# Optimization experiments

Hardware: AMD Instinct MI355X
Metric: run time of the kernel (lower is better)

## Reference

```python
import jax, jax.numpy as jnp
import numpy as np

D = 2048
N_HEADS = 16
N_KV = 4
HEAD_DIM = D // N_HEADS  # 128
N_REP = N_HEADS // N_KV  # 4
B, S = 2, 2048


def setup_inputs() -> dict:
    key = jax.random.key(0)
    ks = jax.random.split(key, 5)
    scale = 0.02
    return {
        "x": jax.random.normal(ks[0], (B, S, D), dtype=jnp.float32),
        "wq": jax.random.normal(ks[1], (D, N_HEADS * HEAD_DIM), dtype=jnp.float32) * scale,
        "wk": jax.random.normal(ks[2], (D, N_KV * HEAD_DIM), dtype=jnp.float32) * scale,
        "wv": jax.random.normal(ks[3], (D, N_KV * HEAD_DIM), dtype=jnp.float32) * scale,
        "wo": jax.random.normal(ks[4], (N_HEADS * HEAD_DIM, D), dtype=jnp.float32) * scale,
    }


def reference(x, wq, wk, wv, wo):
    b, s, _ = x.shape
    # projections
    xq = (x @ wq).reshape(b, s, N_HEADS, HEAD_DIM)
    xk = (x @ wk).reshape(b, s, N_KV, HEAD_DIM)
    xv = (x @ wv).reshape(b, s, N_KV, HEAD_DIM)
    # GQA: group queries per kv head -> [b, n_kv, n_rep, s, d]
    xq = xq.transpose(0, 2, 1, 3).reshape(b, N_KV, N_REP, s, HEAD_DIM)
    xk = xk.transpose(0, 2, 1, 3)  # [b, n_kv, s, d]
    xv = xv.transpose(0, 2, 1, 3)
    scale = 1.0 / jnp.sqrt(jnp.asarray(HEAD_DIM, dtype=x.dtype))
    scores = jnp.einsum('bkrqd,bkvd->bkrqv', xq, xk) * scale  # [b,n_kv,n_rep,s,s]
    causal = jnp.triu(jnp.ones((s, s), dtype=bool), k=1)
    scores = jnp.where(causal, jnp.asarray(-jnp.inf, dtype=scores.dtype), scores)
    probs = jax.nn.softmax(scores, axis=-1)
    out = jnp.einsum('bkrqv,bkvd->bkrqd', probs, xv)  # [b,n_kv,n_rep,s,d]
    out = out.reshape(b, N_HEADS, s, HEAD_DIM).transpose(0, 2, 1, 3).reshape(b, s, N_HEADS * HEAD_DIM)
    return out @ wo
```

## Files before the change

kernel.cpp:

```cpp
#include <hip/hip_runtime.h>

typedef unsigned short u16;
using bf16x8 = __attribute__((ext_vector_type(8))) short;
using bf16x4 = __attribute__((ext_vector_type(4))) short;
using f32x4  = __attribute__((ext_vector_type(4))) float;

#define ATTN_NEG (-3.0e38f)

#if __has_builtin(__builtin_amdgcn_mfma_f32_16x16x16_bf16)
__device__ __forceinline__ f32x4 mfma16(bf16x4 a, bf16x4 b, f32x4 c) {
  return __builtin_amdgcn_mfma_f32_16x16x16_bf16(a, b, c, 0, 0, 0);
}
#elif __has_builtin(__builtin_amdgcn_mfma_f32_16x16x16bf16_1k)
__device__ __forceinline__ f32x4 mfma16(bf16x4 a, bf16x4 b, f32x4 c) {
  return __builtin_amdgcn_mfma_f32_16x16x16bf16_1k(a, b, c, 0, 0, 0);
}
#else
__device__ __forceinline__ f32x4 mfma16(bf16x4 a, bf16x4 b, f32x4 c) {
  asm volatile("v_mfma_f32_16x16x16_bf16 %0, %1, %2, %3"
               : "=v"(c) : "v"(a), "v"(b), "v"(c));
  return c;
}
#endif

__device__ __forceinline__ u16 f2bf_rne(float f) {
  unsigned int u = __float_as_uint(f);
  u += 0x7fffu + ((u >> 16) & 1u);
  return (u16)(u >> 16);
}

__device__ __forceinline__ void load_lds16(const u16* g, u16* l) {
  using gp = const __attribute__((address_space(1))) unsigned int*;
  using lp = __attribute__((address_space(3))) unsigned int*;
  __builtin_amdgcn_global_load_lds((gp)g, (lp)l, 16, 0, 0);
}

__device__ __forceinline__ void transpose_body(const float* __restrict__ in,
                                               u16* __restrict__ out, int K, int N,
                                               int bx, int by, int tid) {
  __shared__ float tile[32][33];
  int tx = tid & 31, ty = tid >> 5;
  int x0 = bx * 32, y0 = by * 32;
  #pragma unroll
  for (int i = 0; i < 32; i += 8)
    tile[ty + i][tx] = in[(size_t)(y0 + ty + i) * N + x0 + tx];
  __syncthreads();
  #pragma unroll
  for (int i = 0; i < 32; i += 8)
    out[(size_t)(x0 + ty + i) * K + y0 + tx] = f2bf_rne(tile[tx][ty + i]);
}

__global__ __launch_bounds__(256) void prep_kernel(const float* __restrict__ x,
                                                   const float* __restrict__ wq,
                                                   const float* __restrict__ wk,
                                                   const float* __restrict__ wv,
                                                   const float* __restrict__ wo,
                                                   u16* xb, u16* wqt, u16* wkt, u16* wvt,
                                                   u16* wot) {
  int bid = blockIdx.x, tid = threadIdx.x;
  if (bid < 8192) {
    int i = bid * 1024 + tid * 4;
    float4 v = *(const float4*)(x + i);
    u16* p = xb + i;
    p[0] = f2bf_rne(v.x); p[1] = f2bf_rne(v.y); p[2] = f2bf_rne(v.z); p[3] = f2bf_rne(v.w);
  } else if (bid < 12288) {
    int t = bid - 8192;
    transpose_body(wq, wqt, 2048, 2048, t & 63, t >> 6, tid);
  } else if (bid < 13312) {
    int t = bid - 12288;
    transpose_body(wk, wkt, 2048, 512, t & 15, t >> 4, tid);
  } else if (bid < 14336) {
    int t = bid - 13312;
    transpose_body(wv, wvt, 2048, 512, t & 15, t >> 4, tid);
  } else {
    int t = bid - 14336;
    transpose_body(wo, wot, 2048, 2048, t & 63, t >> 6, tid);
  }
}

template <int MODE>
__device__ __forceinline__ void gemm_tile(const u16* __restrict__ A, const u16* __restrict__ Bt,
                                          void* __restrict__ Cv, int M, int N, int K,
                                          int bx, int by, char* smem) {
  u16* As = (u16*)smem;
  u16* Bs = (u16*)(smem + 16384);
  const int tid  = threadIdx.x;
  const int wave = tid >> 6, lane = tid & 63;
  const int quad = lane >> 4, l16 = lane & 15;
  const int m0 = by * 128, n0 = bx * 128;
  const int wm = (wave >> 1) * 64, wn = (wave & 1) * 64;
  f32x4 acc[4][4] = {};

  const int srow = lane >> 2;
  const int scol = (lane & 3) << 3;

  for (int k0 = 0; k0 < K; k0 += 64) {
    __syncthreads();
    #pragma unroll
    for (int h = 0; h < 2; ++h)
      #pragma unroll
      for (int i = 0; i < 2; ++i) {
        const int row = wave * 16 + i * 64;
        load_lds16(A  + (size_t)(m0 + row + srow) * K + k0 + h * 32 + scol,
                   As + h * 4096 + row * 32);
        load_lds16(Bt + (size_t)(n0 + row + srow) * K + k0 + h * 32 + scol,
                   Bs + h * 4096 + row * 32);
      }
    __syncthreads();
    #pragma unroll
    for (int h = 0; h < 2; ++h) {
      bf16x8 af[4], bfr[4];
      #pragma unroll
      for (int i = 0; i < 4; ++i) {
        af[i]  = *(const bf16x8*)(As + h * 4096 + (wm + i * 16 + l16) * 32 + quad * 8);
        bfr[i] = *(const bf16x8*)(Bs + h * 4096 + (wn + i * 16 + l16) * 32 + quad * 8);
      }
      #pragma unroll
      for (int mi = 0; mi < 4; ++mi)
        #pragma unroll
        for (int ni = 0; ni < 4; ++ni)
          acc[mi][ni] =
              __builtin_amdgcn_mfma_f32_16x16x32_bf16(af[mi], bfr[ni], acc[mi][ni], 0, 0, 0);
    }
  }

  if constexpr (MODE == 0 || MODE == 3) {
    const float sc = (MODE == 3) ? 0.12751742f : 1.0f;
    u16* Cb = (u16*)Cv;
    #pragma unroll
    for (int mi = 0; mi < 4; ++mi)
      #pragma unroll
      for (int ni = 0; ni < 4; ++ni) {
        int row = m0 + wm + mi * 16 + quad * 4;
        int col = n0 + wn + ni * 16 + l16;
        #pragma unroll
        for (int r = 0; r < 4; ++r)
          Cb[(size_t)(row + r) * N + col] = f2bf_rne(acc[mi][ni][r] * sc);
      }
  } else if constexpr (MODE == 1) {
    u16* Cb = (u16*)Cv;
    #pragma unroll
    for (int mi = 0; mi < 4; ++mi)
      #pragma unroll
      for (int ni = 0; ni < 4; ++ni) {
        int col = n0 + wn + ni * 16 + l16;
        #pragma unroll
        for (int r = 0; r < 4; ++r) {
          int row = m0 + wm + mi * 16 + quad * 4 + r;
          int bb = row >> 11, s = row & 2047;
          int c = s & 31;
          int cp = ((c & 15) >> 2) * 8 + ((c >> 4) & 1) * 4 + (c & 3);
          Cb[((size_t)(bb * 512 + col)) * 2048 + (s & ~31) + cp] = f2bf_rne(acc[mi][ni][r]);
        }
      }
  } else {
    float* Cf = (float*)Cv;
    #pragma unroll
    for (int mi = 0; mi < 4; ++mi)
      #pragma unroll
      for (int ni = 0; ni < 4; ++ni) {
        int row = m0 + wm + mi * 16 + quad * 4;
        int col = n0 + wn + ni * 16 + l16;
        #pragma unroll
        for (int r = 0; r < 4; ++r)
          Cf[(size_t)(row + r) * N + col] = acc[mi][ni][r];
      }
  }
}

__global__ __launch_bounds__(256) void qkv_gemm(const u16* xb, const u16* wqt, const u16* wkt,
                                                const u16* wvt, u16* Qb, u16* Kb, u16* Vt) {
  extern __shared__ char smem[];
  int bx = blockIdx.x, by = blockIdx.y;
  if (bx < 16)
    gemm_tile<3>(xb, wqt, Qb, 4096, 2048, 2048, bx, by, smem);
  else if (bx < 20)
    gemm_tile<0>(xb, wkt, Kb, 4096, 512, 2048, bx - 16, by, smem);
  else
    gemm_tile<1>(xb, wvt, Vt, 4096, 512, 2048, bx - 20, by, smem);
}

template <int MODE>
__global__ __launch_bounds__(256) void gemm_kernel(const u16* A, const u16* Bt, void* C,
                                                   int M, int N, int K) {
  extern __shared__ char smem[];
  gemm_tile<MODE>(A, Bt, C, M, N, K, blockIdx.x, blockIdx.y, smem);
}


__device__ __forceinline__ void stage_kv(const u16* __restrict__ Kg, const u16* __restrict__ Vg,
                                         int kt0, u16* __restrict__ kbuf, u16* __restrict__ vbuf,
                                         int wave, int quad, int l16) {
  #pragma unroll
  for (int h = 0; h < 2; ++h)
    load_lds16(Kg + (size_t)(kt0 + h * 16 + l16) * 512 + wave * 32 + quad * 8,
               kbuf + (wave * 2 + h) * 512);
  #pragma unroll
  for (int i = 0; i < 2; ++i) {
    int f = wave * 2 + i;
    load_lds16(Vg + (size_t)(16 * f + l16) * 2048 + kt0 + quad * 8, vbuf + f * 512);
  }
}

template <bool MASKED>
__device__ __forceinline__ void attn_compute(const u16* __restrict__ kbuf,
                                             const u16* __restrict__ vbuf,
                                             int kt0, int q0w, int quad, int l16,
                                             const bf16x8 (&qf)[4], f32x4 (&o)[8],
                                             float& l_lane) {
  const int slot = (quad * 16 + l16) * 8;
  bf16x8 kf[8];
  #pragma unroll
  for (int kk = 0; kk < 8; ++kk) kf[kk] = *(const bf16x8*)(kbuf + kk * 512 + slot);

  f32x4 sa[2] = {};
  #pragma unroll
  for (int h = 0; h < 2; ++h)
    #pragma unroll
    for (int ks = 0; ks < 4; ++ks)
      sa[h] = __builtin_amdgcn_mfma_f32_16x16x32_bf16(kf[ks * 2 + h], qf[ks], sa[h], 0, 0, 0);

  bf16x4 pa[2];
  #pragma unroll
  for (int h = 0; h < 2; ++h) {
    #pragma unroll
    for (int r = 0; r < 4; ++r) {
      float s = sa[h][r];
      if (MASKED) {
        int kpos = kt0 + 16 * h + quad * 4 + r;
        s = (kpos <= q0w + l16) ? s : ATTN_NEG;
      }
      float p = __builtin_amdgcn_exp2f(s);
      l_lane += p;
      pa[h][r] = (short)f2bf_rne(p);
    }
  }

  #pragma unroll
  for (int f = 0; f < 8; ++f) {
    bf16x8 v8 = *(const bf16x8*)(vbuf + f * 512 + slot);
    bf16x4 vlo = {v8[0], v8[1], v8[2], v8[3]};
    bf16x4 vhi = {v8[4], v8[5], v8[6], v8[7]};
    o[f] = mfma16(pa[0], vlo, o[f]);
    o[f] = mfma16(pa[1], vhi, o[f]);
  }
}

__global__ __launch_bounds__(256, 2) void attn_kernel(const u16* __restrict__ Qb,
                                                      const u16* __restrict__ Kb,
                                                      const u16* __restrict__ Vt,
                                                      u16* __restrict__ Ob) {
  constexpr int S = 2048;
  const int b = blockIdx.z, h = blockIdx.y, g = h >> 2, tp = blockIdx.x;
  const int tid = threadIdx.x;
  const int wave = tid >> 6, lane = tid & 63, quad = lane >> 4, l16 = lane & 15;
  __shared__ alignas(16) u16 Kt[2][4096];
  __shared__ alignas(16) u16 Vl[2][4096];
  __shared__ float lbuf[4][16];

  const u16* Kg = Kb + (size_t)b * S * 512 + g * 128;
  const u16* Vg = Vt + (size_t)(b * 512 + g * 128) * 2048;

  #pragma unroll
  for (int half = 0; half < 2; ++half) {
    const int tile = (half == 0) ? tp : 31 - tp;
    const int wrow = (half == 0) ? wave : 3 - wave;
    const int q0w = tile * 64 + wrow * 16;
    const int nsteps = 2 * tile + 2;
    const int s_diag = 2 * tile + (wrow >> 1);

    bf16x8 qf[4];
    const u16* qrow = Qb + (size_t)(b * S + q0w + l16) * 2048 + h * 128 + quad * 8;
    #pragma unroll
    for (int ks = 0; ks < 4; ++ks) qf[ks] = *(const bf16x8*)(qrow + ks * 32);

    f32x4 o[8] = {};
    float l_lane = 0.f;

    __syncthreads();
    stage_kv(Kg, Vg, 0, Kt[0], Vl[0], wave, quad, l16);

    for (int s = 0; s < nsteps; ++s) {
      __syncthreads();
      if (s + 1 < nsteps)
        stage_kv(Kg, Vg, (s + 1) * 32, Kt[(s + 1) & 1], Vl[(s + 1) & 1], wave, quad, l16);
      if (s < s_diag)
        attn_compute<false>(Kt[s & 1], Vl[s & 1], s * 32, q0w, quad, l16, qf, o, l_lane);
      else if (s == s_diag)
        attn_compute<true>(Kt[s & 1], Vl[s & 1], s * 32, q0w, quad, l16, qf, o, l_lane);
    }

    float lt = l_lane + __shfl_xor(l_lane, 16);
    lt += __shfl_xor(lt, 32);
    if (quad == 0) lbuf[wave][l16] = lt;
    __builtin_amdgcn_wave_barrier();
    float il[4];
    #pragma unroll
    for (int r = 0; r < 4; ++r) il[r] = 1.f / lbuf[wave][quad * 4 + r];

    u16* orow = Ob + (size_t)(b * S + q0w + quad * 4) * 2048 + h * 128 + l16;
    #pragma unroll
    for (int f = 0; f < 8; ++f)
      #pragma unroll
      for (int r = 0; r < 4; ++r)
        orow[(size_t)r * 2048 + f * 16] = f2bf_rne(o[f][r] * il[r]);
  }
}

extern "C" void kernel_launch(void* const* d_in, const int* in_sizes, int n_in,
                              void* d_out, int out_size, void* d_ws, size_t ws_size,
                              hipStream_t stream) {
  const float* x  = (const float*)d_in[0];
  const float* wq = (const float*)d_in[1];
  const float* wk = (const float*)d_in[2];
  const float* wv = (const float*)d_in[3];
  const float* wo = (const float*)d_in[4];
  float* out = (float*)d_out;
  char* ws = (char*)d_ws;

  u16* xb  = (u16*)(ws);
  u16* wqt = (u16*)(ws + 16777216);
  u16* wkt = (u16*)(ws + 25165824);
  u16* wvt = (u16*)(ws + 27262976);
  u16* wot = (u16*)(ws + 29360128);
  u16* Qb  = (u16*)(ws + 37748736);
  u16* Kb  = (u16*)(ws + 54525952);
  u16* Vt  = (u16*)(ws + 58720256);
  u16* Ab  = (u16*)(ws + 62914560);

  prep_kernel<<<18432, 256, 0, stream>>>(x, wq, wk, wv, wo, xb, wqt, wkt, wvt, wot);
  qkv_gemm<<<dim3(24, 32), 256, 32768, stream>>>(xb, wqt, wkt, wvt, Qb, Kb, Vt);
  attn_kernel<<<dim3(16, 16, 2), 256, 0, stream>>>(Qb, Kb, Vt, Ab);
  gemm_kernel<2><<<dim3(16, 32), 256, 32768, stream>>>(Ab, wot, out, 4096, 2048, 2048);
}
```

Baseline: 302.9 us.

## Load V fragments directly from global and use 16x16x32 MFMA for PV

Drops LDS staging of V. Each wave now reads its V fragments straight from global memory (relying on L2/L1 caching), and the two 16x16x16 MFMAs per output fragment become one 16x16x32 MFMA using a packed 8-wide P vector. The grid is also flattened and remapped so consecutive blocks cycle through the 8 (batch, kv-group) pairs, with all heads of a KV group grouped together, presumably to improve L2 locality of shared K/V. This halves the LDS footprint and cuts the V staging traffic, but adds global-load latency on the critical path of each step with no prefetch.

Result: slower. 374.6 us (+23.7%).

```diff
diff --git a/kernel.cpp b/kernel.cpp
--- a/kernel.cpp
+++ b/kernel.cpp
@@ -2,26 +2,9 @@
 
 typedef unsigned short u16;
 using bf16x8 = __attribute__((ext_vector_type(8))) short;
-using bf16x4 = __attribute__((ext_vector_type(4))) short;
 using f32x4  = __attribute__((ext_vector_type(4))) float;
 
 #define ATTN_NEG (-3.0e38f)
-
-#if __has_builtin(__builtin_amdgcn_mfma_f32_16x16x16_bf16)
-__device__ __forceinline__ f32x4 mfma16(bf16x4 a, bf16x4 b, f32x4 c) {
-  return __builtin_amdgcn_mfma_f32_16x16x16_bf16(a, b, c, 0, 0, 0);
-}
-#elif __has_builtin(__builtin_amdgcn_mfma_f32_16x16x16bf16_1k)
-__device__ __forceinline__ f32x4 mfma16(bf16x4 a, bf16x4 b, f32x4 c) {
-  return __builtin_amdgcn_mfma_f32_16x16x16bf16_1k(a, b, c, 0, 0, 0);
-}
-#else
-__device__ __forceinline__ f32x4 mfma16(bf16x4 a, bf16x4 b, f32x4 c) {
-  asm volatile("v_mfma_f32_16x16x16_bf16 %0, %1, %2, %3"
-               : "=v"(c) : "v"(a), "v"(b), "v"(c));
-  return c;
-}
-#endif
 
 __device__ __forceinline__ u16 f2bf_rne(float f) {
   unsigned int u = __float_as_uint(f);
@@ -188,27 +171,26 @@
 }
 
 
-__device__ __forceinline__ void stage_kv(const u16* __restrict__ Kg, const u16* __restrict__ Vg,
-                                         int kt0, u16* __restrict__ kbuf, u16* __restrict__ vbuf,
-                                         int wave, int quad, int l16) {
+__device__ __forceinline__ void stage_k(const u16* __restrict__ Kg, int kt0,
+                                        u16* __restrict__ kbuf, int wave, int quad, int l16) {
   #pragma unroll
   for (int h = 0; h < 2; ++h)
     load_lds16(Kg + (size_t)(kt0 + h * 16 + l16) * 512 + wave * 32 + quad * 8,
                kbuf + (wave * 2 + h) * 512);
-  #pragma unroll
-  for (int i = 0; i < 2; ++i) {
-    int f = wave * 2 + i;
-    load_lds16(Vg + (size_t)(16 * f + l16) * 2048 + kt0 + quad * 8, vbuf + f * 512);
-  }
 }
 
 template <bool MASKED>
 __device__ __forceinline__ void attn_compute(const u16* __restrict__ kbuf,
-                                             const u16* __restrict__ vbuf,
+                                             const u16* __restrict__ Vg,
                                              int kt0, int q0w, int quad, int l16,
                                              const bf16x8 (&qf)[4], f32x4 (&o)[8],
                                              float& l_lane) {
   const int slot = (quad * 16 + l16) * 8;
+  bf16x8 vv[8];
+  #pragma unroll
+  for (int f = 0; f < 8; ++f)
+    vv[f] = *(const bf16x8*)(Vg + (size_t)(16 * f + l16) * 2048 + kt0 + quad * 8);
+
   bf16x8 kf[8];
   #pragma unroll
   for (int kk = 0; kk < 8; ++kk) kf[kk] = *(const bf16x8*)(kbuf + kk * 512 + slot);
@@ -220,9 +202,9 @@
     for (int ks = 0; ks < 4; ++ks)
       sa[h] = __builtin_amdgcn_mfma_f32_16x16x32_bf16(kf[ks * 2 + h], qf[ks], sa[h], 0, 0, 0);
 
-  bf16x4 pa[2];
-  #pragma unroll
-  for (int h = 0; h < 2; ++h) {
+  bf16x8 pc;
+  #pragma unroll
+  for (int h = 0; h < 2; ++h)
     #pragma unroll
     for (int r = 0; r < 4; ++r) {
       float s = sa[h][r];
@@ -232,18 +214,12 @@
       }
       float p = __builtin_amdgcn_exp2f(s);
       l_lane += p;
-      pa[h][r] = (short)f2bf_rne(p);
+      pc[h * 4 + r] = (short)f2bf_rne(p);
     }
-  }
-
-  #pragma unroll
-  for (int f = 0; f < 8; ++f) {
-    bf16x8 v8 = *(const bf16x8*)(vbuf + f * 512 + slot);
-    bf16x4 vlo = {v8[0], v8[1], v8[2], v8[3]};
-    bf16x4 vhi = {v8[4], v8[5], v8[6], v8[7]};
-    o[f] = mfma16(pa[0], vlo, o[f]);
-    o[f] = mfma16(pa[1], vhi, o[f]);
-  }
+
+  #pragma unroll
+  for (int f = 0; f < 8; ++f)
+    o[f] = __builtin_amdgcn_mfma_f32_16x16x32_bf16(pc, vv[f], o[f], 0, 0, 0);
 }
 
 __global__ __launch_bounds__(256, 2) void attn_kernel(const u16* __restrict__ Qb,
@@ -251,11 +227,15 @@
                                                       const u16* __restrict__ Vt,
                                                       u16* __restrict__ Ob) {
   constexpr int S = 2048;
-  const int b = blockIdx.z, h = blockIdx.y, g = h >> 2, tp = blockIdx.x;
+  const int id = blockIdx.x;
+  const int gl = id & 7;
+  const int b = gl >> 2, g = gl & 3;
+  const int loc = id >> 3;
+  const int tp = loc & 15;
+  const int h = g * 4 + (loc >> 4);
   const int tid = threadIdx.x;
   const int wave = tid >> 6, lane = tid & 63, quad = lane >> 4, l16 = lane & 15;
   __shared__ alignas(16) u16 Kt[2][4096];
-  __shared__ alignas(16) u16 Vl[2][4096];
   __shared__ float lbuf[4][16];
 
   const u16* Kg = Kb + (size_t)b * S * 512 + g * 128;
@@ -278,16 +258,16 @@
     float l_lane = 0.f;
 
     __syncthreads();
-    stage_kv(Kg, Vg, 0, Kt[0], Vl[0], wave, quad, l16);
+    stage_k(Kg, 0, Kt[0], wave, quad, l16);
 
     for (int s = 0; s < nsteps; ++s) {
       __syncthreads();
       if (s + 1 < nsteps)
-        stage_kv(Kg, Vg, (s + 1) * 32, Kt[(s + 1) & 1], Vl[(s + 1) & 1], wave, quad, l16);
+        stage_k(Kg, (s + 1) * 32, Kt[(s + 1) & 1], wave, quad, l16);
       if (s < s_diag)
-        attn_compute<false>(Kt[s & 1], Vl[s & 1], s * 32, q0w, quad, l16, qf, o, l_lane);
+        attn_compute<false>(Kt[s & 1], Vg, s * 32, q0w, quad, l16, qf, o, l_lane);
       else if (s == s_diag)
-        attn_compute<true>(Kt[s & 1], Vl[s & 1], s * 32, q0w, quad, l16, qf, o, l_lane);
+        attn_compute<true>(Kt[s & 1], Vg, s * 32, q0w, quad, l16, qf, o, l_lane);
     }
 
     float lt = l_lane + __shfl_xor(l_lane, 16);
@@ -330,6 +310,6 @@
 
   prep_kernel<<<18432, 256, 0, stream>>>(x, wq, wk, wv, wo, xb, wqt, wkt, wvt, wot);
   qkv_gemm<<<dim3(24, 32), 256, 32768, stream>>>(xb, wqt, wkt, wvt, Qb, Kb, Vt);
-  attn_kernel<<<dim3(16, 16, 2), 256, 0, stream>>>(Qb, Kb, Vt, Ab);
+  attn_kernel<<<512, 256, 0, stream>>>(Qb, Kb, Vt, Ab);
   gemm_kernel<2><<<dim3(16, 32), 256, 32768, stream>>>(Ab, wot, out, 4096, 2048, 2048);
 }
```

## Give each attention wave two query sub-tiles and use 16x16x32 MFMA for PV

Applied to the files above, without the earlier changes.

The attention block shrinks from 4 waves to 2, and each wave now processes 32 query rows as two 16-row sub-tiles that share the same K/V fragments read from LDS. This halves LDS reads of K and V per query row. The PV product now uses the 16x16x32 bf16 MFMA on packed 8-wide P and V fragments instead of two 16x16x16 MFMAs. In exchange each wave holds twice as many accumulator and query registers, and there are fewer waves per block, which may reduce latency hiding.

Measured after the change: 347.5 us. 14.7% more time.

```diff
diff --git a/kernel.cpp b/kernel.cpp
--- a/kernel.cpp
+++ b/kernel.cpp
@@ -2,26 +2,9 @@
 
 typedef unsigned short u16;
 using bf16x8 = __attribute__((ext_vector_type(8))) short;
-using bf16x4 = __attribute__((ext_vector_type(4))) short;
 using f32x4  = __attribute__((ext_vector_type(4))) float;
 
 #define ATTN_NEG (-3.0e38f)
-
-#if __has_builtin(__builtin_amdgcn_mfma_f32_16x16x16_bf16)
-__device__ __forceinline__ f32x4 mfma16(bf16x4 a, bf16x4 b, f32x4 c) {
-  return __builtin_amdgcn_mfma_f32_16x16x16_bf16(a, b, c, 0, 0, 0);
-}
-#elif __has_builtin(__builtin_amdgcn_mfma_f32_16x16x16bf16_1k)
-__device__ __forceinline__ f32x4 mfma16(bf16x4 a, bf16x4 b, f32x4 c) {
-  return __builtin_amdgcn_mfma_f32_16x16x16bf16_1k(a, b, c, 0, 0, 0);
-}
-#else
-__device__ __forceinline__ f32x4 mfma16(bf16x4 a, bf16x4 b, f32x4 c) {
-  asm volatile("v_mfma_f32_16x16x16_bf16 %0, %1, %2, %3"
-               : "=v"(c) : "v"(a), "v"(b), "v"(c));
-  return c;
-}
-#endif
 
 __device__ __forceinline__ u16 f2bf_rne(float f) {
   unsigned int u = __float_as_uint(f);
@@ -192,71 +175,77 @@
                                          int kt0, u16* __restrict__ kbuf, u16* __restrict__ vbuf,
                                          int wave, int quad, int l16) {
   #pragma unroll
-  for (int h = 0; h < 2; ++h)
-    load_lds16(Kg + (size_t)(kt0 + h * 16 + l16) * 512 + wave * 32 + quad * 8,
-               kbuf + (wave * 2 + h) * 512);
-  #pragma unroll
-  for (int i = 0; i < 2; ++i) {
-    int f = wave * 2 + i;
+  for (int i = 0; i < 4; ++i) {
+    int kk = wave * 4 + i;
+    load_lds16(Kg + (size_t)(kt0 + 16 * (kk & 1) + l16) * 512 + (kk >> 1) * 32 + quad * 8,
+               kbuf + kk * 512);
+  }
+  #pragma unroll
+  for (int i = 0; i < 4; ++i) {
+    int f = wave * 4 + i;
     load_lds16(Vg + (size_t)(16 * f + l16) * 2048 + kt0 + quad * 8, vbuf + f * 512);
   }
 }
 
 template <bool MASKED>
-__device__ __forceinline__ void attn_compute(const u16* __restrict__ kbuf,
-                                             const u16* __restrict__ vbuf,
-                                             int kt0, int q0w, int quad, int l16,
-                                             const bf16x8 (&qf)[4], f32x4 (&o)[8],
-                                             float& l_lane) {
+__device__ __forceinline__ void attn_compute2(const u16* __restrict__ kbuf,
+                                              const u16* __restrict__ vbuf,
+                                              int kt0, int q0w, int quad, int l16,
+                                              const bf16x8 (&qfa)[4], const bf16x8 (&qfb)[4],
+                                              f32x4 (&oa)[8], f32x4 (&ob)[8],
+                                              float& la, float& lb) {
   const int slot = (quad * 16 + l16) * 8;
   bf16x8 kf[8];
   #pragma unroll
   for (int kk = 0; kk < 8; ++kk) kf[kk] = *(const bf16x8*)(kbuf + kk * 512 + slot);
 
-  f32x4 sa[2] = {};
+  f32x4 sa[2] = {}, sb[2] = {};
   #pragma unroll
   for (int h = 0; h < 2; ++h)
     #pragma unroll
-    for (int ks = 0; ks < 4; ++ks)
-      sa[h] = __builtin_amdgcn_mfma_f32_16x16x32_bf16(kf[ks * 2 + h], qf[ks], sa[h], 0, 0, 0);
-
-  bf16x4 pa[2];
-  #pragma unroll
-  for (int h = 0; h < 2; ++h) {
+    for (int ks = 0; ks < 4; ++ks) {
+      sa[h] = __builtin_amdgcn_mfma_f32_16x16x32_bf16(kf[ks * 2 + h], qfa[ks], sa[h], 0, 0, 0);
+      sb[h] = __builtin_amdgcn_mfma_f32_16x16x32_bf16(kf[ks * 2 + h], qfb[ks], sb[h], 0, 0, 0);
+    }
+
+  bf16x8 pca, pcb;
+  #pragma unroll
+  for (int h = 0; h < 2; ++h)
     #pragma unroll
     for (int r = 0; r < 4; ++r) {
-      float s = sa[h][r];
+      int kpos = kt0 + 16 * h + quad * 4 + r;
+      float s0 = sa[h][r], s1 = sb[h][r];
       if (MASKED) {
-        int kpos = kt0 + 16 * h + quad * 4 + r;
-        s = (kpos <= q0w + l16) ? s : ATTN_NEG;
-      }
-      float p = __builtin_amdgcn_exp2f(s);
-      l_lane += p;
-      pa[h][r] = (short)f2bf_rne(p);
-    }
-  }
+        s0 = (kpos <= q0w + l16) ? s0 : ATTN_NEG;
+        s1 = (kpos <= q0w + 16 + l16) ? s1 : ATTN_NEG;
+      }
+      float p0 = __builtin_amdgcn_exp2f(s0);
+      float p1 = __builtin_amdgcn_exp2f(s1);
+      la += p0;
+      lb += p1;
+      pca[h * 4 + r] = (short)f2bf_rne(p0);
+      pcb[h * 4 + r] = (short)f2bf_rne(p1);
+    }
 
   #pragma unroll
   for (int f = 0; f < 8; ++f) {
     bf16x8 v8 = *(const bf16x8*)(vbuf + f * 512 + slot);
-    bf16x4 vlo = {v8[0], v8[1], v8[2], v8[3]};
-    bf16x4 vhi = {v8[4], v8[5], v8[6], v8[7]};
-    o[f] = mfma16(pa[0], vlo, o[f]);
-    o[f] = mfma16(pa[1], vhi, o[f]);
-  }
-}
-
-__global__ __launch_bounds__(256, 2) void attn_kernel(const u16* __restrict__ Qb,
-                                                      const u16* __restrict__ Kb,
-                                                      const u16* __restrict__ Vt,
-                                                      u16* __restrict__ Ob) {
+    oa[f] = __builtin_amdgcn_mfma_f32_16x16x32_bf16(pca, v8, oa[f], 0, 0, 0);
+    ob[f] = __builtin_amdgcn_mfma_f32_16x16x32_bf16(pcb, v8, ob[f], 0, 0, 0);
+  }
+}
+
+__global__ __launch_bounds__(128) void attn_kernel(const u16* __restrict__ Qb,
+                                                   const u16* __restrict__ Kb,
+                                                   const u16* __restrict__ Vt,
+                                                   u16* __restrict__ Ob) {
   constexpr int S = 2048;
   const int b = blockIdx.z, h = blockIdx.y, g = h >> 2, tp = blockIdx.x;
   const int tid = threadIdx.x;
   const int wave = tid >> 6, lane = tid & 63, quad = lane >> 4, l16 = lane & 15;
   __shared__ alignas(16) u16 Kt[2][4096];
   __shared__ alignas(16) u16 Vl[2][4096];
-  __shared__ float lbuf[4][16];
+  __shared__ float lbuf[2][2][16];
 
   const u16* Kg = Kb + (size_t)b * S * 512 + g * 128;
   const u16* Vg = Vt + (size_t)(b * 512 + g * 128) * 2048;
@@ -264,18 +253,22 @@
   #pragma unroll
   for (int half = 0; half < 2; ++half) {
     const int tile = (half == 0) ? tp : 31 - tp;
-    const int wrow = (half == 0) ? wave : 3 - wave;
-    const int q0w = tile * 64 + wrow * 16;
+    const int wrow = (half == 0) ? wave : 1 - wave;
+    const int q0w = tile * 64 + wrow * 32;
     const int nsteps = 2 * tile + 2;
-    const int s_diag = 2 * tile + (wrow >> 1);
-
-    bf16x8 qf[4];
-    const u16* qrow = Qb + (size_t)(b * S + q0w + l16) * 2048 + h * 128 + quad * 8;
-    #pragma unroll
-    for (int ks = 0; ks < 4; ++ks) qf[ks] = *(const bf16x8*)(qrow + ks * 32);
-
-    f32x4 o[8] = {};
-    float l_lane = 0.f;
+    const int s_diag = 2 * tile + wrow;
+
+    bf16x8 qfa[4], qfb[4];
+    const u16* qra = Qb + (size_t)(b * S + q0w + l16) * 2048 + h * 128 + quad * 8;
+    const u16* qrb = qra + (size_t)16 * 2048;
+    #pragma unroll
+    for (int ks = 0; ks < 4; ++ks) {
+      qfa[ks] = *(const bf16x8*)(qra + ks * 32);
+      qfb[ks] = *(const bf16x8*)(qrb + ks * 32);
+    }
+
+    f32x4 oa[8] = {}, ob[8] = {};
+    float la = 0.f, lb = 0.f;
 
     __syncthreads();
     stage_kv(Kg, Vg, 0, Kt[0], Vl[0], wave, quad, l16);
@@ -285,25 +278,38 @@
       if (s + 1 < nsteps)
         stage_kv(Kg, Vg, (s + 1) * 32, Kt[(s + 1) & 1], Vl[(s + 1) & 1], wave, quad, l16);
       if (s < s_diag)
-        attn_compute<false>(Kt[s & 1], Vl[s & 1], s * 32, q0w, quad, l16, qf, o, l_lane);
+        attn_compute2<false>(Kt[s & 1], Vl[s & 1], s * 32, q0w, quad, l16, qfa, qfb, oa, ob,
+                             la, lb);
       else if (s == s_diag)
-        attn_compute<true>(Kt[s & 1], Vl[s & 1], s * 32, q0w, quad, l16, qf, o, l_lane);
-    }
-
-    float lt = l_lane + __shfl_xor(l_lane, 16);
-    lt += __shfl_xor(lt, 32);
-    if (quad == 0) lbuf[wave][l16] = lt;
+        attn_compute2<true>(Kt[s & 1], Vl[s & 1], s * 32, q0w, quad, l16, qfa, qfb, oa, ob,
+                            la, lb);
+    }
+
+    float lta = la + __shfl_xor(la, 16);
+    lta += __shfl_xor(lta, 32);
+    float ltb = lb + __shfl_xor(lb, 16);
+    ltb += __shfl_xor(ltb, 32);
+    if (quad == 0) {
+      lbuf[wave][0][l16] = lta;
+      lbuf[wave][1][l16] = ltb;
+    }
     __builtin_amdgcn_wave_barrier();
-    float il[4];
-    #pragma unroll
-    for (int r = 0; r < 4; ++r) il[r] = 1.f / lbuf[wave][quad * 4 + r];
-
-    u16* orow = Ob + (size_t)(b * S + q0w + quad * 4) * 2048 + h * 128 + l16;
+    float ila[4], ilb[4];
+    #pragma unroll
+    for (int r = 0; r < 4; ++r) {
+      ila[r] = 1.f / lbuf[wave][0][quad * 4 + r];
+      ilb[r] = 1.f / lbuf[wave][1][quad * 4 + r];
+    }
+
+    u16* ora = Ob + (size_t)(b * S + q0w + quad * 4) * 2048 + h * 128 + l16;
+    u16* orb = ora + (size_t)16 * 2048;
     #pragma unroll
     for (int f = 0; f < 8; ++f)
       #pragma unroll
-      for (int r = 0; r < 4; ++r)
-        orow[(size_t)r * 2048 + f * 16] = f2bf_rne(o[f][r] * il[r]);
+      for (int r = 0; r < 4; ++r) {
+        ora[(size_t)r * 2048 + f * 16] = f2bf_rne(oa[f][r] * ila[r]);
+        orb[(size_t)r * 2048 + f * 16] = f2bf_rne(ob[f][r] * ilb[r]);
+      }
   }
 }
 
@@ -330,6 +336,6 @@
 
   prep_kernel<<<18432, 256, 0, stream>>>(x, wq, wk, wv, wo, xb, wqt, wkt, wvt, wot);
   qkv_gemm<<<dim3(24, 32), 256, 32768, stream>>>(xb, wqt, wkt, wvt, Qb, Kb, Vt);
-  attn_kernel<<<dim3(16, 16, 2), 256, 0, stream>>>(Qb, Kb, Vt, Ab);
+  attn_kernel<<<dim3(16, 16, 2), 128, 0, stream>>>(Qb, Kb, Vt, Ab);
   gemm_kernel<2><<<dim3(16, 32), 256, 32768, stream>>>(Ab, wot, out, 4096, 2048, 2048);
 }
```

## Triple-buffer K/V staging, use 16x16x32 MFMA for PV, add setprio

Applied to the files above, without the earlier changes.

Moves the K/V LDS staging from a double to a triple buffer with two tiles prefetched ahead. Each step now waits on a partial vmcnt plus a raw s_barrier instead of a full __syncthreads, so global loads can overlap more compute. The PV product now uses one 16x16x32 bf16 MFMA per output fragment instead of two 16x16x16 ones, which drops the vector repacking. MFMA sections are wrapped in s_setprio raises. The cost is 50% more LDS, which could limit occupancy, plus redundant loads of the last tile near the end of the loop and fragile hand-tuned vmcnt counts.

Result: no change. 306.7 us (+1.3%).

```diff
diff --git a/kernel.cpp b/kernel.cpp
--- a/kernel.cpp
+++ b/kernel.cpp
@@ -2,26 +2,9 @@
 
 typedef unsigned short u16;
 using bf16x8 = __attribute__((ext_vector_type(8))) short;
-using bf16x4 = __attribute__((ext_vector_type(4))) short;
 using f32x4  = __attribute__((ext_vector_type(4))) float;
 
 #define ATTN_NEG (-3.0e38f)
-
-#if __has_builtin(__builtin_amdgcn_mfma_f32_16x16x16_bf16)
-__device__ __forceinline__ f32x4 mfma16(bf16x4 a, bf16x4 b, f32x4 c) {
-  return __builtin_amdgcn_mfma_f32_16x16x16_bf16(a, b, c, 0, 0, 0);
-}
-#elif __has_builtin(__builtin_amdgcn_mfma_f32_16x16x16bf16_1k)
-__device__ __forceinline__ f32x4 mfma16(bf16x4 a, bf16x4 b, f32x4 c) {
-  return __builtin_amdgcn_mfma_f32_16x16x16bf16_1k(a, b, c, 0, 0, 0);
-}
-#else
-__device__ __forceinline__ f32x4 mfma16(bf16x4 a, bf16x4 b, f32x4 c) {
-  asm volatile("v_mfma_f32_16x16x16_bf16 %0, %1, %2, %3"
-               : "=v"(c) : "v"(a), "v"(b), "v"(c));
-  return c;
-}
-#endif
 
 __device__ __forceinline__ u16 f2bf_rne(float f) {
   unsigned int u = __float_as_uint(f);
@@ -214,15 +197,17 @@
   for (int kk = 0; kk < 8; ++kk) kf[kk] = *(const bf16x8*)(kbuf + kk * 512 + slot);
 
   f32x4 sa[2] = {};
+  __builtin_amdgcn_s_setprio(1);
   #pragma unroll
   for (int h = 0; h < 2; ++h)
     #pragma unroll
     for (int ks = 0; ks < 4; ++ks)
       sa[h] = __builtin_amdgcn_mfma_f32_16x16x32_bf16(kf[ks * 2 + h], qf[ks], sa[h], 0, 0, 0);
-
-  bf16x4 pa[2];
-  #pragma unroll
-  for (int h = 0; h < 2; ++h) {
+  __builtin_amdgcn_s_setprio(0);
+
+  bf16x8 pc;
+  #pragma unroll
+  for (int h = 0; h < 2; ++h)
     #pragma unroll
     for (int r = 0; r < 4; ++r) {
       float s = sa[h][r];
@@ -232,18 +217,16 @@
       }
       float p = __builtin_amdgcn_exp2f(s);
       l_lane += p;
-      pa[h][r] = (short)f2bf_rne(p);
+      pc[h * 4 + r] = (short)f2bf_rne(p);
     }
-  }
-
+
+  __builtin_amdgcn_s_setprio(1);
   #pragma unroll
   for (int f = 0; f < 8; ++f) {
     bf16x8 v8 = *(const bf16x8*)(vbuf + f * 512 + slot);
-    bf16x4 vlo = {v8[0], v8[1], v8[2], v8[3]};
-    bf16x4 vhi = {v8[4], v8[5], v8[6], v8[7]};
-    o[f] = mfma16(pa[0], vlo, o[f]);
-    o[f] = mfma16(pa[1], vhi, o[f]);
-  }
+    o[f] = __builtin_amdgcn_mfma_f32_16x16x32_bf16(pc, v8, o[f], 0, 0, 0);
+  }
+  __builtin_amdgcn_s_setprio(0);
 }
 
 __global__ __launch_bounds__(256, 2) void attn_kernel(const u16* __restrict__ Qb,
@@ -254,14 +237,13 @@
   const int b = blockIdx.z, h = blockIdx.y, g = h >> 2, tp = blockIdx.x;
   const int tid = threadIdx.x;
   const int wave = tid >> 6, lane = tid & 63, quad = lane >> 4, l16 = lane & 15;
-  __shared__ alignas(16) u16 Kt[2][4096];
-  __shared__ alignas(16) u16 Vl[2][4096];
+  __shared__ alignas(16) u16 Kt[3][4096];
+  __shared__ alignas(16) u16 Vl[3][4096];
   __shared__ float lbuf[4][16];
 
   const u16* Kg = Kb + (size_t)b * S * 512 + g * 128;
   const u16* Vg = Vt + (size_t)(b * 512 + g * 128) * 2048;
 
-  #pragma unroll
   for (int half = 0; half < 2; ++half) {
     const int tile = (half == 0) ? tp : 31 - tp;
     const int wrow = (half == 0) ? wave : 3 - wave;
@@ -273,22 +255,33 @@
     const u16* qrow = Qb + (size_t)(b * S + q0w + l16) * 2048 + h * 128 + quad * 8;
     #pragma unroll
     for (int ks = 0; ks < 4; ++ks) qf[ks] = *(const bf16x8*)(qrow + ks * 32);
+    asm volatile("s_waitcnt vmcnt(0)" ::: "memory");
+    #pragma unroll
+    for (int ks = 0; ks < 4; ++ks)
+      asm volatile("" : "+v"(qf[ks]));
 
     f32x4 o[8] = {};
     float l_lane = 0.f;
 
     __syncthreads();
     stage_kv(Kg, Vg, 0, Kt[0], Vl[0], wave, quad, l16);
+    stage_kv(Kg, Vg, 32, Kt[1], Vl[1], wave, quad, l16);
 
     for (int s = 0; s < nsteps; ++s) {
-      __syncthreads();
-      if (s + 1 < nsteps)
-        stage_kv(Kg, Vg, (s + 1) * 32, Kt[(s + 1) & 1], Vl[(s + 1) & 1], wave, quad, l16);
+      asm volatile("s_waitcnt vmcnt(4)" ::: "memory");
+      __builtin_amdgcn_s_barrier();
+      {
+        const int sn = (s + 2 < nsteps) ? s + 2 : nsteps - 1;
+        const int bn = (s + 2) % 3;
+        stage_kv(Kg, Vg, sn * 32, Kt[bn], Vl[bn], wave, quad, l16);
+      }
+      const int bc = s % 3;
       if (s < s_diag)
-        attn_compute<false>(Kt[s & 1], Vl[s & 1], s * 32, q0w, quad, l16, qf, o, l_lane);
+        attn_compute<false>(Kt[bc], Vl[bc], s * 32, q0w, quad, l16, qf, o, l_lane);
       else if (s == s_diag)
-        attn_compute<true>(Kt[s & 1], Vl[s & 1], s * 32, q0w, quad, l16, qf, o, l_lane);
+        attn_compute<true>(Kt[bc], Vl[bc], s * 32, q0w, quad, l16, qf, o, l_lane);
     }
+    asm volatile("s_waitcnt vmcnt(0)" ::: "memory");
 
     float lt = l_lane + __shfl_xor(l_lane, 16);
     lt += __shfl_xor(lt, 32);
```
